# Kernel optimization log

Hardware: AMD Instinct MI355X
Metric: run time of the kernel (lower is better)

Reference implementation:

```python
import jax, jax.numpy as jnp
import numpy as np

B, N, C_IN, C_OUT = 16, 1024, 256, 256
POOL_RATIO = 0.5  # pooling_ration


def setup_inputs() -> dict:
    key = jax.random.key(0)
    k0, k1, k2, k3 = jax.random.split(key, 4)
    x = jax.random.normal(k0, (B, N, C_IN), dtype=jnp.float32)
    # sparse-ish dense adjacency (as the module stores adj densely)
    adj = (jax.random.uniform(k1, (B, N, N)) < 0.02).astype(jnp.float32)
    mask = jnp.ones((B, N), dtype=jnp.int32)
    n_nodes = jnp.full((B,), N, dtype=jnp.int32)
    stdv = 1.0 / np.sqrt(C_IN)
    W = jax.random.uniform(k2, (C_IN, C_OUT), minval=-stdv, maxval=stdv, dtype=jnp.float32)
    b = jnp.zeros((C_OUT,), dtype=jnp.float32)
    pooling = jax.random.uniform(k3, (C_OUT, 1), minval=-1.0, maxval=1.0, dtype=jnp.float32)
    return {"x": x, "adj": adj, "mask": mask, "n_nodes": n_nodes, "W": W, "b": b, "pooling": pooling}


def reference(x, adj, mask, n_nodes, W, b, pooling):
    # GraphConvolutionLayer: adj @ (x W) + b   (standard Kipf GCN layer)
    h = jnp.einsum('bnm,bmc->bnc', adj, x @ W) + b          # [B,N,C_OUT]
    Bm, Nm, C = h.shape
    # projection score y = (h @ pooling) / ||pooling||
    y = (h.reshape(Bm * Nm, C) @ pooling).reshape(Bm, Nm)
    y = y / jnp.sqrt(jnp.sum(pooling ** 2))
    # ascending sort indices
    idx = jnp.argsort(y, axis=1)                            # [B,N]
    n_remove = (n_nodes.astype(jnp.float32) * (1.0 - POOL_RATIO)).astype(jnp.int32)
    new_n_nodes = n_nodes - n_remove
    # vectorized equivalent of the per-batch loop: among currently-masked nodes
    # (in ascending-score order), zero out the first n_remove[b] of them.
    m_sorted = jnp.take_along_axis(mask, idx, axis=1)       # mask gathered in sorted order
    rank = jnp.cumsum(m_sorted, axis=1) - m_sorted          # exclusive rank among masked
    remove = (m_sorted == 1) & (rank < n_remove[:, None])
    new_sorted = jnp.where(remove, 0, m_sorted)
    inv = jnp.argsort(idx, axis=1)                          # inverse permutation
    new_mask = jnp.take_along_axis(new_sorted, inv, axis=1)  # [B,N] int
    mf = new_mask.astype(h.dtype)
    x_out = h * jnp.tanh(y)[:, :, None] * mf[:, :, None]
    adj_out = mf[:, :, None] * adj * mf[:, None, :]
    return x_out, adj_out, new_mask, new_n_nodes
```

## Files before the change

kernel.cpp:

```cpp
#include <hip/hip_runtime.h>
#include <math.h>

#define Bsz 16
#define Nn  1024

#define ADJ_OFF    (16*1024*256)
#define MASK_OFF   (ADJ_OFF + 16*1024*1024)
#define NN_OFF     (MASK_OFF + 16*1024)

typedef unsigned long long u64;
typedef unsigned short u16;
typedef short bf16x8 __attribute__((ext_vector_type(8)));
typedef float f32x4  __attribute__((ext_vector_type(4)));

static __device__ inline u16 f2bf(float f) {
    unsigned u = __float_as_uint(f);
    u += 0x7fffu + ((u >> 16) & 1u);
    return (u16)(u >> 16);
}

static __device__ inline u64 spread4(u64 x) {
    x &= 0xFFFFULL;
    x = (x | (x << 24)) & 0x000000FF000000FFULL;
    x = (x | (x << 12)) & 0x000F000F000F000FULL;
    x = (x | (x << 6))  & 0x0303030303030303ULL;
    x = (x | (x << 3))  & 0x1111111111111111ULL;
    return x;
}

static __device__ inline bf16x8 expand8(unsigned kb) {
    union { unsigned u[4]; bf16x8 v; } r;
    #pragma unroll
    for (int p = 0; p < 4; ++p) {
        unsigned lo = (kb >> (2 * p)) & 1u;
        unsigned hi = (kb >> (2 * p + 1)) & 1u;
        r.u[p] = (lo ? 0x3F80u : 0u) | (hi ? 0x3F800000u : 0u);
    }
    return r.v;
}

__global__ __launch_bounds__(256) void k1(const float* __restrict__ x,
                                          const float* __restrict__ W,
                                          const float* __restrict__ pool,
                                          u16* __restrict__ XB,
                                          u16* __restrict__ WT,
                                          float* __restrict__ Z) {
    int bid = blockIdx.x, t = threadIdx.x, lane = t & 63, wid = t >> 6;
    if (bid < 256) {
        __shared__ float sp[256];
        __shared__ float swp[256];
        sp[t] = pool[t];
        __syncthreads();
        float acc = 0.f;
        const float* wr = W + t * 256;
        for (int j = 0; j < 256; j += 4) {
            float4 w4 = *(const float4*)&wr[j];
            acc = fmaf(w4.x, sp[j], fmaf(w4.y, sp[j + 1],
                  fmaf(w4.z, sp[j + 2], fmaf(w4.w, sp[j + 3], acc))));
        }
        swp[t] = acc;
        __syncthreads();
        const float* w4p = &swp[lane * 4];
        float wx = w4p[0], wy = w4p[1], wz = w4p[2], ww = w4p[3];
        int base = bid * 64 + wid * 16;
        #pragma unroll 1
        for (int rb = 0; rb < 4; ++rb) {
            float4 v[4];
            #pragma unroll
            for (int k = 0; k < 4; ++k)
                v[k] = ((const float4*)(x + (size_t)(base + rb * 4 + k) * 256))[lane];
            #pragma unroll
            for (int k = 0; k < 4; ++k) {
                int row = base + rb * 4 + k;
                ushort4 o;
                o.x = f2bf(v[k].x); o.y = f2bf(v[k].y); o.z = f2bf(v[k].z); o.w = f2bf(v[k].w);
                ((ushort4*)(XB + (size_t)row * 256))[lane] = o;
                float a = fmaf(v[k].x, wx, fmaf(v[k].y, wy, fmaf(v[k].z, wz, v[k].w * ww)));
                for (int off = 32; off > 0; off >>= 1) a += __shfl_down(a, off, 64);
                if (lane == 0) Z[row] = a;
            }
        }
    } else {
        __shared__ float sT[64][65];
        int bt = bid - 256;
        int tr = (bt >> 2) * 64, tc = (bt & 3) * 64;
        #pragma unroll
        for (int p = 0; p < 4; ++p) {
            int r = p * 16 + (t >> 4), c = (t & 15) * 4;
            float4 w = *(const float4*)&W[(size_t)(tr + r) * 256 + tc + c];
            sT[r][c] = w.x; sT[r][c + 1] = w.y; sT[r][c + 2] = w.z; sT[r][c + 3] = w.w;
        }
        __syncthreads();
        #pragma unroll
        for (int p = 0; p < 2; ++p) {
            int nl = p * 32 + (t >> 3), kl = (t & 7) * 8;
            u16 tmp[8];
            #pragma unroll
            for (int j = 0; j < 8; ++j) tmp[j] = f2bf(sT[kl + j][nl]);
            *(int4*)&WT[(size_t)(tc + nl) * 256 + tr + kl] = *(const int4*)tmp;
        }
    }
}

__global__ __launch_bounds__(256) void k2(const u16* __restrict__ XB,
                                          const u16* __restrict__ WT,
                                          const float* __restrict__ adj,
                                          const float* __restrict__ Z,
                                          u16* __restrict__ XWBT,
                                          u64* __restrict__ ABITS,
                                          float* __restrict__ Y) {
    int t = threadIdx.x, lane = t & 63, wid = t >> 6;
    if (blockIdx.x < 256) {
        __shared__ __align__(16) short smem[2 * 128 * 72];
        short (*sA)[72] = (short (*)[72])smem;
        short (*sB)[72] = (short (*)[72])(smem + 128 * 72);
        int idx = blockIdx.x;
        int b  = (idx & 7) + ((idx >> 7) << 3);
        int tl = (idx >> 3) & 15;
        int bm = (b << 3) + (tl >> 1);
        int bn = tl & 1;
        int wr = (wid >> 1) * 64, wc = (wid & 1) * 64;
        int fm = lane & 15, fq = lane >> 4;

        f32x4 acc[4][4];
        #pragma unroll
        for (int i = 0; i < 4; ++i)
            #pragma unroll
            for (int j = 0; j < 4; ++j)
                acc[i][j] = (f32x4){0.f, 0.f, 0.f, 0.f};

        int sr = t >> 1, half = (t & 1) * 32;
        const u16* gA = XB + ((size_t)(bm * 128 + sr)) * 256 + half;
        const u16* gB = WT + ((size_t)(bn * 128 + sr)) * 256 + half;

        for (int kt = 0; kt < 4; ++kt) {
            __syncthreads();
            #pragma unroll
            for (int q = 0; q < 4; ++q) {
                *(int4*)&sA[sr][half + q * 8] = *(const int4*)&gA[kt * 64 + q * 8];
                *(int4*)&sB[sr][half + q * 8] = *(const int4*)&gB[kt * 64 + q * 8];
            }
            __syncthreads();
            #pragma unroll
            for (int ks = 0; ks < 64; ks += 32) {
                bf16x8 af[4], bfv[4];
                #pragma unroll
                for (int i = 0; i < 4; ++i)
                    af[i] = *(const bf16x8*)&sA[wr + i * 16 + fm][ks + fq * 8];
                #pragma unroll
                for (int j = 0; j < 4; ++j)
                    bfv[j] = *(const bf16x8*)&sB[wc + j * 16 + fm][ks + fq * 8];
                __builtin_amdgcn_s_setprio(1);
                #pragma unroll
                for (int i = 0; i < 4; ++i)
                    #pragma unroll
                    for (int j = 0; j < 4; ++j)
                        acc[i][j] = __builtin_amdgcn_mfma_f32_16x16x32_bf16(af[i], bfv[j], acc[i][j], 0, 0, 0);
                __builtin_amdgcn_s_setprio(0);
            }
        }
        __syncthreads();
        short (*sT)[136] = (short (*)[136])smem;
        #pragma unroll
        for (int i = 0; i < 4; ++i) {
            int m = wr + i * 16 + fq * 4;
            #pragma unroll
            for (int j = 0; j < 4; ++j) {
                int c = wc + j * 16 + fm;
                #pragma unroll
                for (int r = 0; r < 4; ++r)
                    sT[c][m + r] = (short)f2bf(acc[i][j][r]);
            }
        }
        __syncthreads();
        u16* dst = XWBT + (size_t)b * 262144 + (size_t)(bn * 128) * 1024 + (bm & 7) * 128;
        int cl = t >> 4, mo = (t & 15) * 8;
        #pragma unroll
        for (int p = 0; p < 8; ++p) {
            int c = p * 16 + cl;
            *(int4*)&dst[(size_t)c * 1024 + mo] = *(const int4*)&sT[c][mo];
        }
    } else {
        int g = blockIdx.x - 256;
        int b = (g & 7) + ((g >> 9) << 3);
        int grp = (g >> 3) & 63;
        __shared__ float sZ[1024];
        ((float4*)sZ)[t] = ((const float4*)(Z + (b << 10)))[t];
        __syncthreads();
        const float* z0 = &sZ[lane * 4];
        #pragma unroll 1
        for (int rr = 0; rr < 4; ++rr) {
            int row = (b << 10) + grp * 16 + wid * 4 + rr;
            const float4* ar = (const float4*)(adj + (size_t)row * 1024);
            float4 v0 = ar[lane], v1 = ar[64 + lane], v2 = ar[128 + lane], v3 = ar[192 + lane];
            u64 B00 = __ballot(v0.x != 0.f), B01 = __ballot(v0.y != 0.f);
            u64 B02 = __ballot(v0.z != 0.f), B03 = __ballot(v0.w != 0.f);
            u64 B10 = __ballot(v1.x != 0.f), B11 = __ballot(v1.y != 0.f);
            u64 B12 = __ballot(v1.z != 0.f), B13 = __ballot(v1.w != 0.f);
            u64 B20 = __ballot(v2.x != 0.f), B21 = __ballot(v2.y != 0.f);
            u64 B22 = __ballot(v2.z != 0.f), B23 = __ballot(v2.w != 0.f);
            u64 B30 = __ballot(v3.x != 0.f), B31 = __ballot(v3.y != 0.f);
            u64 B32 = __ballot(v3.z != 0.f), B33 = __ballot(v3.w != 0.f);
            u64 t0, t1, t2, t3;
            int c = (lane >> 2) & 3;
            if (c == 0)      { t0 = B00; t1 = B01; t2 = B02; t3 = B03; }
            else if (c == 1) { t0 = B10; t1 = B11; t2 = B12; t3 = B13; }
            else if (c == 2) { t0 = B20; t1 = B21; t2 = B22; t3 = B23; }
            else             { t0 = B30; t1 = B31; t2 = B32; t3 = B33; }
            int sh = (lane & 3) * 16;
            u64 wbits = spread4(t0 >> sh) | (spread4(t1 >> sh) << 1)
                      | (spread4(t2 >> sh) << 2) | (spread4(t3 >> sh) << 3);
            if (lane < 16) ABITS[(size_t)row * 16 + lane] = wbits;
            float a = v0.x * z0[0] + v0.y * z0[1] + v0.z * z0[2] + v0.w * z0[3];
            a += v1.x * z0[256] + v1.y * z0[257] + v1.z * z0[258] + v1.w * z0[259];
            a += v2.x * z0[512] + v2.y * z0[513] + v2.z * z0[514] + v2.w * z0[515];
            a += v3.x * z0[768] + v3.y * z0[769] + v3.z * z0[770] + v3.w * z0[771];
            for (int off = 32; off > 0; off >>= 1) a += __shfl_down(a, off, 64);
            if (lane == 0) Y[row] = a;
        }
    }
}

__global__ __launch_bounds__(256) void k3(const float* __restrict__ Y,
                                          const int* __restrict__ maskIn,
                                          const int* __restrict__ nNodes,
                                          const float* __restrict__ bias,
                                          const float* __restrict__ pool,
                                          float* __restrict__ SCALE,
                                          float* __restrict__ NM,
                                          float* __restrict__ newN,
                                          u64* __restrict__ NMBITS) {
    __shared__ u64 sKey[1024];
    __shared__ float redb[4], redq[4];

    int bid = blockIdx.x;
    int b = bid >> 2, chunk = bid & 3;
    int t = threadIdx.x, lane = t & 63, wid = t >> 6;
    int base = b << 10;

    {
        float pv = pool[t];
        float bv = bias[t] * pv;
        float qv = pv * pv;
        for (int off = 32; off > 0; off >>= 1) {
            bv += __shfl_down(bv, off, 64);
            qv += __shfl_down(qv, off, 64);
        }
        if (lane == 0) { redb[wid] = bv; redq[wid] = qv; }
    }

    #pragma unroll
    for (int p = 0; p < 4; ++p) {
        int i = p * 256 + t;
        unsigned u = __float_as_uint(Y[base + i]);
        u = (u & 0x80000000u) ? ~u : (u | 0x80000000u);
        int m = maskIn[base + i];
        sKey[i] = ((u64)u << 32) | (unsigned)(i | (m << 16));
    }
    __syncthreads();

    float sBP  = redb[0] + redb[1] + redb[2] + redb[3];
    float sINV = 1.0f / sqrtf(redq[0] + redq[1] + redq[2] + redq[3]);

    int i = chunk * 256 + t;
    u64 ki = sKey[i];
    int rank = 0;
    #pragma unroll 8
    for (int j = 0; j < 1024; j += 2) {
        u64 k0 = sKey[j], k1 = sKey[j + 1];
        rank += ((k0 < ki) && ((unsigned)(k0 >> 16) & 1u)) ? 1 : 0;
        rank += ((k1 < ki) && ((unsigned)(k1 >> 16) & 1u)) ? 1 : 0;
    }

    int mi = (int)((unsigned)(ki >> 16) & 1u);
    int nn = nNodes[b];
    int nrem = (int)((float)nn * 0.5f);
    int nm = (mi == 1 && rank < nrem) ? 0 : mi;
    NM[base + i] = (float)nm;
    u64 bmask = __ballot(nm != 0);
    if (lane == 0) NMBITS[b * 16 + chunk * 4 + wid] = bmask;
    float yr = Y[base + i];
    SCALE[base + i] = nm ? tanhf((yr + sBP) * sINV) : 0.0f;
    if (chunk == 0 && t == 0) newN[b] = (float)(nn - nrem);
}

__global__ __launch_bounds__(256) void k4(const u64* __restrict__ ABITS,
                                          const u16* __restrict__ XWBT,
                                          const float* __restrict__ SCALE,
                                          const float* __restrict__ bias,
                                          const u64* __restrict__ NMBITS,
                                          float* __restrict__ XO,
                                          float* __restrict__ AO) {
    int t = threadIdx.x, lane = t & 63, wid = t >> 6;
    if (blockIdx.x < 256) {
        __shared__ u64 sBitsA[128][18];
        __shared__ short sB[128][72];
        int idx = blockIdx.x;
        int b   = (idx & 7) + ((idx >> 7) << 3);
        int tl  = (idx >> 3) & 15;
        int bmt = tl >> 1, bn = tl & 1;
        int wr = (wid >> 1) * 64, wc = (wid & 1) * 64;
        int fm = lane & 15, fq = lane >> 4;

        {
            int r = t >> 1, hq = (t & 1) * 8;
            const u64* src = ABITS + ((size_t)(b * 1024 + bmt * 128 + r)) * 16 + hq;
            #pragma unroll
            for (int q = 0; q < 8; q += 2) {
                ulonglong2 v = *(const ulonglong2*)&src[q];
                sBitsA[r][hq + q] = v.x;
                sBitsA[r][hq + q + 1] = v.y;
            }
        }

        f32x4 acc[4][4];
        #pragma unroll
        for (int i = 0; i < 4; ++i)
            #pragma unroll
            for (int j = 0; j < 4; ++j)
                acc[i][j] = (f32x4){0.f, 0.f, 0.f, 0.f};

        int sr = t >> 1, half = (t & 1) * 32;
        const u16* gB = XWBT + (size_t)b * 262144 + (size_t)(bn * 128 + sr) * 1024 + half;
        __syncthreads();

        for (int kt = 0; kt < 16; ++kt) {
            __syncthreads();
            #pragma unroll
            for (int q = 0; q < 4; ++q)
                *(int4*)&sB[sr][half + q * 8] = *(const int4*)&gB[kt * 64 + q * 8];
            __syncthreads();
            u64 rb[4];
            #pragma unroll
            for (int i = 0; i < 4; ++i)
                rb[i] = sBitsA[wr + i * 16 + fm][kt];
            #pragma unroll
            for (int ks = 0; ks < 64; ks += 32) {
                bf16x8 af[4], bfv[4];
                #pragma unroll
                for (int i = 0; i < 4; ++i)
                    af[i] = expand8((unsigned)(rb[i] >> (ks + fq * 8)) & 0xFFu);
                #pragma unroll
                for (int j = 0; j < 4; ++j)
                    bfv[j] = *(const bf16x8*)&sB[wc + j * 16 + fm][ks + fq * 8];
                __builtin_amdgcn_s_setprio(1);
                #pragma unroll
                for (int i = 0; i < 4; ++i)
                    #pragma unroll
                    for (int j = 0; j < 4; ++j)
                        acc[i][j] = __builtin_amdgcn_mfma_f32_16x16x32_bf16(af[i], bfv[j], acc[i][j], 0, 0, 0);
                __builtin_amdgcn_s_setprio(0);
            }
        }
        float bj[4];
        #pragma unroll
        for (int j = 0; j < 4; ++j) bj[j] = bias[bn * 128 + wc + j * 16 + fm];
        int mb = (b << 10) + bmt * 128 + wr;
        #pragma unroll
        for (int i = 0; i < 4; ++i) {
            int m0 = mb + i * 16 + fq * 4;
            float s0 = SCALE[m0], s1 = SCALE[m0 + 1], s2 = SCALE[m0 + 2], s3 = SCALE[m0 + 3];
            #pragma unroll
            for (int j = 0; j < 4; ++j) {
                int c = bn * 128 + wc + j * 16 + fm;
                float* xo = XO + (size_t)m0 * 256 + c;
                xo[0]   = (acc[i][j][0] + bj[j]) * s0;
                xo[256] = (acc[i][j][1] + bj[j]) * s1;
                xo[512] = (acc[i][j][2] + bj[j]) * s2;
                xo[768] = (acc[i][j][3] + bj[j]) * s3;
            }
        }
    } else {
        int g = blockIdx.x - 256;
        int b = (g & 7) + ((g >> 9) << 3);
        int grp = (g >> 3) & 63;
        __shared__ u64 sNMB[16];
        __shared__ u64 sRB[16][17];
        if (t < 16) sNMB[t] = NMBITS[b * 16 + t];
        sRB[t >> 4][t & 15] = ABITS[((size_t)((b << 10) + grp * 16 + (t >> 4))) * 16 + (t & 15)];
        __syncthreads();
        int c0 = t * 4;
        u64 wb = sNMB[c0 >> 6] >> (c0 & 63);
        float m0 = (wb & 1) ? 1.f : 0.f;
        float m1 = ((wb >> 1) & 1) ? 1.f : 0.f;
        float m2 = ((wb >> 2) & 1) ? 1.f : 0.f;
        float m3 = ((wb >> 3) & 1) ? 1.f : 0.f;
        #pragma unroll 1
        for (int r = 0; r < 16; ++r) {
            int rloc = grp * 16 + r;
            int nmRow = (int)((sNMB[rloc >> 6] >> (rloc & 63)) & 1ULL);
            float4* aor = (float4*)(AO + (size_t)((b << 10) + rloc) * 1024);
            if (nmRow) {
                unsigned rbits = (unsigned)(sRB[r][t >> 4] >> (4 * (t & 15))) & 0xFu;
                float4 o;
                o.x = (rbits & 1u) ? m0 : 0.f;
                o.y = (rbits & 2u) ? m1 : 0.f;
                o.z = (rbits & 4u) ? m2 : 0.f;
                o.w = (rbits & 8u) ? m3 : 0.f;
                aor[t] = o;
            } else {
                aor[t] = make_float4(0.f, 0.f, 0.f, 0.f);
            }
        }
    }
}

extern "C" void kernel_launch(void* const* d_in, const int* in_sizes, int n_in,
                              void* d_out, int out_size, void* d_ws, size_t ws_size,
                              hipStream_t stream) {
    const float* x      = (const float*)d_in[0];
    const float* adj    = (const float*)d_in[1];
    const int*   mask   = (const int*)d_in[2];
    const int*   nnodes = (const int*)d_in[3];
    const float* W      = (const float*)d_in[4];
    const float* bias   = (const float*)d_in[5];
    const float* pool   = (const float*)d_in[6];

    float* out = (float*)d_out;
    float* XO  = out;
    float* AO  = out + ADJ_OFF;
    float* NM  = out + MASK_OFF;
    float* NNo = out + NN_OFF;

    char* w = (char*)d_ws;
    u16*   XB     = (u16*)(w);
    u16*   WT     = (u16*)(w + 8388608);
    u16*   XWBT   = (u16*)(w + 8519680);
    u64*   ABITS  = (u64*)(w + 16908288);
    float* Z      = (float*)(w + 19005440);
    float* Y      = (float*)(w + 19070976);
    float* SCALE  = (float*)(w + 19136512);
    u64*   NMBITS = (u64*)(w + 19202048);

    k1<<<272, 256, 0, stream>>>(x, W, pool, XB, WT, Z);
    k2<<<1280, 256, 0, stream>>>(XB, WT, adj, Z, XWBT, ABITS, Y);
    k3<<<64, 256, 0, stream>>>(Y, mask, nnodes, bias, pool, SCALE, NM, NNo, NMBITS);
    k4<<<1280, 256, 0, stream>>>(ABITS, XWBT, SCALE, bias, NMBITS, XO, AO);
}
```

Baseline: 216.7 us.

## Fuse mask ranking into final kernel via per-block bitonic sort

Removes the separate ranking kernel and has every block of the output kernel recompute the sorted order of scores with a shared-memory bitonic sort, followed by a prefix scan over the mask. The new mask and tanh scale stay in shared memory instead of passing through global buffers. This saves a launch and a round trip through global memory. In exchange, each of the 1280 blocks repeats the same sort with many barriers.

After: 216.1 us. Within noise of the previous version (-0.3%).

```diff
diff --git a/kernel.cpp b/kernel.cpp
--- a/kernel.cpp
+++ b/kernel.cpp
@@ -221,21 +221,40 @@
     }
 }
 
-__global__ __launch_bounds__(256) void k3(const float* __restrict__ Y,
+__global__ __launch_bounds__(256) void k4(const u64* __restrict__ ABITS,
+                                          const u16* __restrict__ XWBT,
+                                          const float* __restrict__ Y,
                                           const int* __restrict__ maskIn,
                                           const int* __restrict__ nNodes,
                                           const float* __restrict__ bias,
                                           const float* __restrict__ pool,
-                                          float* __restrict__ SCALE,
                                           float* __restrict__ NM,
                                           float* __restrict__ newN,
-                                          u64* __restrict__ NMBITS) {
-    __shared__ u64 sKey[1024];
+                                          float* __restrict__ XO,
+                                          float* __restrict__ AO) {
+    __shared__ __align__(16) unsigned char smem[36864];
+    __shared__ float sScale[128];
+    __shared__ int   wsum[4];
     __shared__ float redb[4], redq[4];
 
-    int bid = blockIdx.x;
-    int b = bid >> 2, chunk = bid & 3;
+    u64 (*sBitsA)[18] = (u64 (*)[18])smem;
+    short (*sB)[72]   = (short (*)[72])(smem + 18432);
+    u64*  sk    = (u64*)(smem + 18432);
+    int*  nmLoc = (int*)(smem + 18432 + 8192);
+    u64 (*sRB)[17] = (u64 (*)[17])smem;
+
     int t = threadIdx.x, lane = t & 63, wid = t >> 6;
+    bool isGemm = blockIdx.x < 256;
+    int b, tl = 0, bmt = 0, bn = 0, grp = 0;
+    if (isGemm) {
+        int idx = blockIdx.x;
+        b = (idx & 7) + ((idx >> 7) << 3);
+        tl = (idx >> 3) & 15; bmt = tl >> 1; bn = tl & 1;
+    } else {
+        int g = blockIdx.x - 256;
+        b = (g & 7) + ((g >> 9) << 3);
+        grp = (g >> 3) & 63;
+    }
     int base = b << 10;
 
     {
@@ -248,71 +267,96 @@
         }
         if (lane == 0) { redb[wid] = bv; redq[wid] = qv; }
     }
-
     #pragma unroll
     for (int p = 0; p < 4; ++p) {
         int i = p * 256 + t;
         unsigned u = __float_as_uint(Y[base + i]);
         u = (u & 0x80000000u) ? ~u : (u | 0x80000000u);
-        int m = maskIn[base + i];
-        sKey[i] = ((u64)u << 32) | (unsigned)(i | (m << 16));
+        sk[i] = ((u64)u << 32) | (unsigned)i;
+    }
+    if (isGemm) {
+        int r = t >> 1, hq = (t & 1) * 8;
+        const u64* src = ABITS + ((size_t)(b * 1024 + bmt * 128 + r)) * 16 + hq;
+        #pragma unroll
+        for (int q = 0; q < 8; q += 2) {
+            ulonglong2 v = *(const ulonglong2*)&src[q];
+            sBitsA[r][hq + q] = v.x;
+            sBitsA[r][hq + q + 1] = v.y;
+        }
+    } else {
+        sRB[t >> 4][t & 15] = ABITS[((size_t)(base + grp * 16 + (t >> 4))) * 16 + (t & 15)];
     }
     __syncthreads();
-
     float sBP  = redb[0] + redb[1] + redb[2] + redb[3];
     float sINV = 1.0f / sqrtf(redq[0] + redq[1] + redq[2] + redq[3]);
 
-    int i = chunk * 256 + t;
-    u64 ki = sKey[i];
-    int rank = 0;
-    #pragma unroll 8
-    for (int j = 0; j < 1024; j += 2) {
-        u64 k0 = sKey[j], k1 = sKey[j + 1];
-        rank += ((k0 < ki) && ((unsigned)(k0 >> 16) & 1u)) ? 1 : 0;
-        rank += ((k1 < ki) && ((unsigned)(k1 >> 16) & 1u)) ? 1 : 0;
-    }
-
-    int mi = (int)((unsigned)(ki >> 16) & 1u);
-    int nn = nNodes[b];
-    int nrem = (int)((float)nn * 0.5f);
-    int nm = (mi == 1 && rank < nrem) ? 0 : mi;
-    NM[base + i] = (float)nm;
-    u64 bmask = __ballot(nm != 0);
-    if (lane == 0) NMBITS[b * 16 + chunk * 4 + wid] = bmask;
-    float yr = Y[base + i];
-    SCALE[base + i] = nm ? tanhf((yr + sBP) * sINV) : 0.0f;
-    if (chunk == 0 && t == 0) newN[b] = (float)(nn - nrem);
-}
-
-__global__ __launch_bounds__(256) void k4(const u64* __restrict__ ABITS,
-                                          const u16* __restrict__ XWBT,
-                                          const float* __restrict__ SCALE,
-                                          const float* __restrict__ bias,
-                                          const u64* __restrict__ NMBITS,
-                                          float* __restrict__ XO,
-                                          float* __restrict__ AO) {
-    int t = threadIdx.x, lane = t & 63, wid = t >> 6;
-    if (blockIdx.x < 256) {
-        __shared__ u64 sBitsA[128][18];
-        __shared__ short sB[128][72];
-        int idx = blockIdx.x;
-        int b   = (idx & 7) + ((idx >> 7) << 3);
-        int tl  = (idx >> 3) & 15;
-        int bmt = tl >> 1, bn = tl & 1;
+    for (int k = 2; k <= 1024; k <<= 1) {
+        for (int j = k >> 1; j >= 1; j >>= 1) {
+            #pragma unroll
+            for (int p = 0; p < 2; ++p) {
+                int q = p * 256 + t;
+                int i = ((q & ~(j - 1)) << 1) | (q & (j - 1));
+                int ip = i | j;
+                bool up = ((i & k) == 0);
+                u64 a = sk[i], c = sk[ip];
+                if ((a > c) == up) { sk[i] = c; sk[ip] = a; }
+            }
+            __syncthreads();
+        }
+    }
+
+    {
+        int m[4], id4[4], ts = 0;
+        #pragma unroll
+        for (int s = 0; s < 4; ++s) {
+            u64 v = sk[4 * t + s];
+            int id = (int)(v & 1023u);
+            id4[s] = id;
+            int mm = maskIn[base + id];
+            m[s] = mm; ts += mm;
+        }
+        int sc = ts;
+        for (int off = 1; off < 64; off <<= 1) {
+            int nv = __shfl_up(sc, off, 64);
+            if (lane >= off) sc += nv;
+        }
+        if (lane == 63) wsum[wid] = sc;
+        __syncthreads();
+        int offset = 0;
+        for (int w = 0; w < wid; ++w) offset += wsum[w];
+        int run = sc - ts + offset;
+        int nn = nNodes[b];
+        int nrem = (int)((float)nn * 0.5f);
+        #pragma unroll
+        for (int s = 0; s < 4; ++s) {
+            int nm = (m[s] == 1 && run < nrem) ? 0 : m[s];
+            run += m[s];
+            nmLoc[id4[s]] = nm;
+        }
+        __syncthreads();
+
+        if (isGemm) {
+            if (t < 128) {
+                int node = bmt * 128 + t;
+                int nm = nmLoc[node];
+                float yv = Y[base + node];
+                sScale[t] = nm ? tanhf((yv + sBP) * sINV) : 0.0f;
+            }
+            if (tl == 0) {
+                #pragma unroll
+                for (int p = 0; p < 4; ++p) {
+                    int node = p * 256 + t;
+                    NM[base + node] = (float)nmLoc[node];
+                }
+                if (t == 0) newN[b] = (float)(nn - nrem);
+            }
+        }
+    }
+
+    if (isGemm) {
         int wr = (wid >> 1) * 64, wc = (wid & 1) * 64;
         int fm = lane & 15, fq = lane >> 4;
 
-        {
-            int r = t >> 1, hq = (t & 1) * 8;
-            const u64* src = ABITS + ((size_t)(b * 1024 + bmt * 128 + r)) * 16 + hq;
-            #pragma unroll
-            for (int q = 0; q < 8; q += 2) {
-                ulonglong2 v = *(const ulonglong2*)&src[q];
-                sBitsA[r][hq + q] = v.x;
-                sBitsA[r][hq + q + 1] = v.y;
-            }
-        }
-
         f32x4 acc[4][4];
         #pragma unroll
         for (int i = 0; i < 4; ++i)
@@ -322,7 +366,6 @@
 
         int sr = t >> 1, half = (t & 1) * 32;
         const u16* gB = XWBT + (size_t)b * 262144 + (size_t)(bn * 128 + sr) * 1024 + half;
-        __syncthreads();
 
         for (int kt = 0; kt < 16; ++kt) {
             __syncthreads();
@@ -355,11 +398,12 @@
         float bj[4];
         #pragma unroll
         for (int j = 0; j < 4; ++j) bj[j] = bias[bn * 128 + wc + j * 16 + fm];
-        int mb = (b << 10) + bmt * 128 + wr;
+        int mb = base + bmt * 128 + wr;
         #pragma unroll
         for (int i = 0; i < 4; ++i) {
+            int lrow = wr + i * 16 + fq * 4;
             int m0 = mb + i * 16 + fq * 4;
-            float s0 = SCALE[m0], s1 = SCALE[m0 + 1], s2 = SCALE[m0 + 2], s3 = SCALE[m0 + 3];
+            float s0 = sScale[lrow], s1 = sScale[lrow + 1], s2 = sScale[lrow + 2], s3 = sScale[lrow + 3];
             #pragma unroll
             for (int j = 0; j < 4; ++j) {
                 int c = bn * 128 + wc + j * 16 + fm;
@@ -371,25 +415,16 @@
             }
         }
     } else {
-        int g = blockIdx.x - 256;
-        int b = (g & 7) + ((g >> 9) << 3);
-        int grp = (g >> 3) & 63;
-        __shared__ u64 sNMB[16];
-        __shared__ u64 sRB[16][17];
-        if (t < 16) sNMB[t] = NMBITS[b * 16 + t];
-        sRB[t >> 4][t & 15] = ABITS[((size_t)((b << 10) + grp * 16 + (t >> 4))) * 16 + (t & 15)];
-        __syncthreads();
         int c0 = t * 4;
-        u64 wb = sNMB[c0 >> 6] >> (c0 & 63);
-        float m0 = (wb & 1) ? 1.f : 0.f;
-        float m1 = ((wb >> 1) & 1) ? 1.f : 0.f;
-        float m2 = ((wb >> 2) & 1) ? 1.f : 0.f;
-        float m3 = ((wb >> 3) & 1) ? 1.f : 0.f;
+        float m0 = nmLoc[c0]     ? 1.f : 0.f;
+        float m1 = nmLoc[c0 + 1] ? 1.f : 0.f;
+        float m2 = nmLoc[c0 + 2] ? 1.f : 0.f;
+        float m3 = nmLoc[c0 + 3] ? 1.f : 0.f;
         #pragma unroll 1
         for (int r = 0; r < 16; ++r) {
             int rloc = grp * 16 + r;
-            int nmRow = (int)((sNMB[rloc >> 6] >> (rloc & 63)) & 1ULL);
-            float4* aor = (float4*)(AO + (size_t)((b << 10) + rloc) * 1024);
+            int nmRow = nmLoc[rloc];
+            float4* aor = (float4*)(AO + (size_t)(base + rloc) * 1024);
             if (nmRow) {
                 unsigned rbits = (unsigned)(sRB[r][t >> 4] >> (4 * (t & 15))) & 0xFu;
                 float4 o;
@@ -429,11 +464,8 @@
     u64*   ABITS  = (u64*)(w + 16908288);
     float* Z      = (float*)(w + 19005440);
     float* Y      = (float*)(w + 19070976);
-    float* SCALE  = (float*)(w + 19136512);
-    u64*   NMBITS = (u64*)(w + 19202048);
 
     k1<<<272, 256, 0, stream>>>(x, W, pool, XB, WT, Z);
     k2<<<1280, 256, 0, stream>>>(XB, WT, adj, Z, XWBT, ABITS, Y);
-    k3<<<64, 256, 0, stream>>>(Y, mask, nnodes, bias, pool, SCALE, NM, NNo, NMBITS);
-    k4<<<1280, 256, 0, stream>>>(ABITS, XWBT, SCALE, bias, NMBITS, XO, AO);
-}
+    k4<<<1280, 256, 0, stream>>>(ABITS, XWBT, Y, mask, nnodes, bias, pool, NM, NNo, XO, AO);
+}
```
